# Performance work log

Hardware: AMD Instinct MI355X
Metric: run time of the kernel (lower is better)

## Reference

```python
import jax, jax.numpy as jnp
import numpy as np

N = 100000   # nodes
E = 1600000  # edges (avg degree 16)
IN = 128; HID = 128; OUT = 128; HEADS = 4
C = HID // HEADS  # 32 per-head channels


def setup_inputs() -> dict:
    key = jax.random.key(0)
    ks = jax.random.split(key, 16)
    inp = {
        "x": jax.random.normal(ks[0], (N, IN), jnp.float32),
        "edge_index": jax.random.randint(ks[1], (2, E), 0, N, dtype=jnp.int64),
        # layer 0: GATConv(IN -> C, heads=4), concat -> HID
        "W0": jax.random.normal(ks[2], (IN, HEADS * C), jnp.float32) * 0.1,
        "as0": jax.random.normal(ks[3], (HEADS, C), jnp.float32) * 0.1,
        "ad0": jax.random.normal(ks[4], (HEADS, C), jnp.float32) * 0.1,
        "b0": jax.random.normal(ks[5], (HEADS * C,), jnp.float32) * 0.1,
        # layer 1: GATConv(HID -> C, heads=4), concat -> HID
        "W1": jax.random.normal(ks[6], (HID, HEADS * C), jnp.float32) * 0.1,
        "as1": jax.random.normal(ks[7], (HEADS, C), jnp.float32) * 0.1,
        "ad1": jax.random.normal(ks[8], (HEADS, C), jnp.float32) * 0.1,
        "b1": jax.random.normal(ks[9], (HEADS * C,), jnp.float32) * 0.1,
        # layer 2: GATConv(HID -> OUT, heads=1)
        "W2": jax.random.normal(ks[10], (HID, OUT), jnp.float32) * 0.1,
        "as2": jax.random.normal(ks[11], (1, OUT), jnp.float32) * 0.1,
        "ad2": jax.random.normal(ks[12], (1, OUT), jnp.float32) * 0.1,
        "b2": jax.random.normal(ks[13], (OUT,), jnp.float32) * 0.1,
    }
    return inp


def _gat_layer(h, src, dst, W, a_src, a_dst, b, n):
    """PyG-style GATConv (concat=True, negative_slope=0.2, self-loops already in src/dst)."""
    heads, c = a_src.shape
    g = (h @ W).reshape(n, heads, c)                      # [N,H,C]
    al = jnp.sum(g * a_src, axis=-1)                      # [N,H] source attention term
    ar = jnp.sum(g * a_dst, axis=-1)                      # [N,H] dest attention term
    e = jax.nn.leaky_relu(al[src] + ar[dst], 0.2)         # [Etot,H]
    # segment softmax over incoming edges of each dst node (stable)
    m = jax.ops.segment_max(e, dst, num_segments=n)
    ex = jnp.exp(e - m[dst])
    s = jax.ops.segment_sum(ex, dst, num_segments=n)
    alpha = ex / (s[dst] + 1e-16)                         # [Etot,H]
    out = jax.ops.segment_sum(g[src] * alpha[..., None], dst, num_segments=n)  # [N,H,C]
    return out.reshape(n, heads * c) + b


def reference(x, edge_index, W0, as0, ad0, b0, W1, as1, ad1, b1, W2, as2, ad2, b2):
    n = x.shape[0]
    loops = jnp.arange(n, dtype=edge_index.dtype)         # add_self_loops=True
    src = jnp.concatenate([edge_index[0], loops])
    dst = jnp.concatenate([edge_index[1], loops])
    h = jax.nn.relu(_gat_layer(x, src, dst, W0, as0, ad0, b0, n))  # dropout inactive (eval)
    h = jax.nn.relu(_gat_layer(h, src, dst, W1, as1, ad1, b1, n))
    return _gat_layer(h, src, dst, W2, as2, ad2, b2, n)
```

## Files before the change

### kernel.cpp

```cpp
#include <hip/hip_runtime.h>
#include <hip/hip_bf16.h>
#include <hip/hip_fp16.h>

#define NNODES 100000
#define NEDGES 1600000
#define ETOT   (NEDGES + NNODES)
#define SCANB  1024
#define NSCAN  ((NNODES + SCANB - 1) / SCANB)
#define NB     782
#define NBINBLK 256

typedef _Float16 half8 __attribute__((ext_vector_type(8)));
typedef float f32x4 __attribute__((ext_vector_type(4)));

struct WSrc { const void* p[12]; };

__device__ __forceinline__ float ld_f(const void* p, long i, int f32) {
  if (f32) return ((const float*)p)[i];
  return __bfloat162float(((const __hip_bfloat16*)p)[i]);
}

__device__ __forceinline__ unsigned short f2bf_bits(float v) {
  __hip_bfloat16 b = __float2bfloat16(v);
  return __builtin_bit_cast(unsigned short, b);
}

__global__ void detect_kernel(const void* xraw, const void* eraw, int* flags) {
  __shared__ int cnt0, cnt1;
  if (threadIdx.x == 0) { cnt0 = 0; cnt1 = 0; }
  __syncthreads();
  const int* e32 = (const int*)eraw;
  int nz = 0;
  for (int i = threadIdx.x; i < 2048; i += blockDim.x) nz += (e32[2 * i + 1] != 0);
  const unsigned short* xs = (const unsigned short*)xraw;
  int weird = 0;
  for (int i = threadIdx.x; i < 4096; i += blockDim.x) {
    unsigned short u = xs[2 * i];
    int ex = (u >> 7) & 0xFF;
    weird += (ex > 168 || (ex < 88 && ex != 0)) ? 1 : 0;
  }
  atomicAdd(&cnt0, nz);
  atomicAdd(&cnt1, weird);
  __syncthreads();
  if (threadIdx.x == 0) {
    flags[0] = (cnt0 < 1024) ? 1 : 0;
    flags[1] = (cnt1 > 512) ? 1 : 0;
  }
}

__global__ void conv_wts_kernel(WSrc wsrc, float* dst, const int* flags) {
  const int start[13] = {0, 16384, 16512, 16640, 16768, 33152, 33280, 33408,
                         33536, 49920, 50048, 50176, 50304};
  int f32 = flags[1];
  int stride = gridDim.x * blockDim.x;
  for (int i = blockIdx.x * blockDim.x + threadIdx.x; i < 50304; i += stride) {
    int s = 0;
    while (start[s + 1] <= i) s++;
    dst[i] = ld_f(wsrc.p[s], i - start[s], f32);
  }
}

__global__ void conv_wtrans(const float* wts, __half* Wt) {
  const int woff[3] = {0, 16768, 33536};
  int i = blockIdx.x * blockDim.x + threadIdx.x;
  if (i >= 3 * 16384) return;
  int layer = i >> 14, rem = i & 16383;
  int c = rem >> 7, k = rem & 127;
  Wt[i] = __float2half(wts[woff[layer] + k * 128 + c]);
}

__device__ __forceinline__ void load_edge(const void* raw, int i64, long e, int& s, int& d) {
  if (i64) {
    const long long* r = (const long long*)raw;
    s = (int)r[e];
    d = (int)r[NEDGES + e];
  } else {
    const int* r = (const int*)raw;
    s = r[e];
    d = r[NEDGES + e];
  }
}

__device__ __forceinline__ int load_dst(const void* raw, int i64, long e) {
  if (i64) return (int)((const long long*)raw)[NEDGES + e];
  return ((const int*)raw)[NEDGES + e];
}

__global__ __launch_bounds__(256) void binhist(const void* raw, const int* flags, int* bcnt) {
  __shared__ int h[NB];
  for (int t = threadIdx.x; t < NB; t += 256) h[t] = 0;
  __syncthreads();
  int i64 = flags[0];
  long per = (NEDGES + NBINBLK - 1) / NBINBLK;
  long lo = (long)blockIdx.x * per;
  long hi = lo + per; if (hi > NEDGES) hi = NEDGES;
  for (long e = lo + threadIdx.x; e < hi; e += 256)
    atomicAdd(&h[load_dst(raw, i64, e) >> 7], 1);
  __syncthreads();
  for (int t = threadIdx.x; t < NB; t += 256) {
    int c = h[t];
    if (c) atomicAdd(&bcnt[t], c);
  }
}

__global__ __launch_bounds__(1024) void binscan(const int* bcnt, int* boff, int* bcur) {
  __shared__ int lds[1024];
  int t = threadIdx.x;
  int x = (t < NB) ? bcnt[t] : 0;
  lds[t] = x;
  __syncthreads();
  for (int off = 1; off < 1024; off <<= 1) {
    int v = (t >= off) ? lds[t - off] : 0;
    __syncthreads();
    lds[t] += v;
    __syncthreads();
  }
  int excl = lds[t] - x;
  if (t < NB) { boff[t] = excl; bcur[t] = excl; }
  if (t == 0) boff[NB] = NEDGES;
}

__global__ __launch_bounds__(256) void binplace(const void* raw, const int* flags, int* bcur,
                                                int* ebuf) {
  __shared__ int hist[NB];
  __shared__ int base[NB];
  int i64 = flags[0];
  long per = (NEDGES + NBINBLK - 1) / NBINBLK;
  long lo = (long)blockIdx.x * per;
  long hi = lo + per; if (hi > NEDGES) hi = NEDGES;
  for (int t = threadIdx.x; t < NB; t += 256) hist[t] = 0;
  __syncthreads();
  for (long e = lo + threadIdx.x; e < hi; e += 256)
    atomicAdd(&hist[load_dst(raw, i64, e) >> 7], 1);
  __syncthreads();
  for (int t = threadIdx.x; t < NB; t += 256) {
    int c = hist[t];
    base[t] = c ? atomicAdd(&bcur[t], c) : 0;
    hist[t] = 0;
  }
  __syncthreads();
  for (long e = lo + threadIdx.x; e < hi; e += 256) {
    int s, d;
    load_edge(raw, i64, e, s, d);
    int b = d >> 7;
    int pos = base[b] + atomicAdd(&hist[b], 1);
    ebuf[pos] = s | ((d & 127) << 17);
  }
}

__global__ __launch_bounds__(256) void deghist(const int* ebuf, const int* boff, int* deg) {
  __shared__ int h[128];
  int b = blockIdx.x, t = threadIdx.x;
  if (t < 128) h[t] = 0;
  __syncthreads();
  int beg = boff[b], end = boff[b + 1];
  for (int i = beg + t; i < end; i += 256) atomicAdd(&h[ebuf[i] >> 17], 1);
  __syncthreads();
  int node = b * 128 + t;
  if (t < 128 && node < NNODES) deg[node] = h[t];
}

__global__ __launch_bounds__(1024) void scan_part(const int* deg, int* part) {
  __shared__ int lds[SCANB];
  int b = blockIdx.x, t = threadIdx.x;
  int idx = b * SCANB + t;
  lds[t] = (idx < NNODES) ? deg[idx] + 1 : 0;
  __syncthreads();
  for (int off = 512; off > 0; off >>= 1) {
    if (t < off) lds[t] += lds[t + off];
    __syncthreads();
  }
  if (t == 0) part[b] = lds[0];
}

__global__ __launch_bounds__(128) void scan_tops(int* part) {
  __shared__ int lds[128];
  int t = threadIdx.x;
  lds[t] = (t < NSCAN) ? part[t] : 0;
  __syncthreads();
  for (int off = 1; off < 128; off <<= 1) {
    int v = (t >= off) ? lds[t - off] : 0;
    __syncthreads();
    lds[t] += v;
    __syncthreads();
  }
  if (t < NSCAN) part[t] = (t == 0) ? 0 : lds[t - 1];
}

__global__ __launch_bounds__(1024) void scan_write(const int* deg, const int* part, int* rs) {
  __shared__ int lds[SCANB];
  int b = blockIdx.x, t = threadIdx.x;
  int idx = b * SCANB + t;
  int x = (idx < NNODES) ? deg[idx] + 1 : 0;
  lds[t] = x;
  __syncthreads();
  for (int off = 1; off < SCANB; off <<= 1) {
    int v = (t >= off) ? lds[t - off] : 0;
    __syncthreads();
    lds[t] += v;
    __syncthreads();
  }
  int incl = part[b] + lds[t];
  int excl = incl - x;
  if (idx < NNODES) rs[idx] = excl;
  if (idx == NNODES - 1) rs[NNODES] = incl;
}

__global__ __launch_bounds__(256) void bucket_scatter(const int* ebuf, const int* boff,
                                                      const int* rs, int* adj) {
  __shared__ int cur[128];
  int b = blockIdx.x, t = threadIdx.x;
  int node = b * 128 + t;
  if (t < 128) cur[t] = (node < NNODES) ? rs[node] : 0;
  __syncthreads();
  int beg = boff[b], end = boff[b + 1];
  for (int i = beg + t; i < end; i += 256) {
    int v = ebuf[i];
    int pos = atomicAdd(&cur[v >> 17], 1);
    adj[pos] = v & 0x1FFFF;
  }
  __syncthreads();
  if (t < 128 && node < NNODES) adj[cur[t]] = node;
}

template <int H, int SRC>
__global__ __launch_bounds__(256) void gemm_mfma(const void* Araw, const float* wts,
                                                 const __half* Wt, int as_off, int ad_off,
                                                 __half* G, float* al, float* ar,
                                                 const int* flags) {
  __shared__ unsigned short Wl[128 * 128];
  __shared__ unsigned short Al[64 * 128];
  const int tid = threadIdx.x;
  const int rowbase = blockIdx.x * 64;
  for (int i = tid; i < 2048; i += 256) {
    int col = i >> 4, kc = i & 15;
    ((uint4*)Wl)[col * 16 + (kc ^ (col & 7))] = ((const uint4*)Wt)[i];
  }
  if (SRC == 0) {
    const __half* A = (const __half*)Araw;
    for (int i = tid; i < 1024; i += 256) {
      int row = i >> 4, kc = i & 15;
      int grow = rowbase + row;
      uint4 v = {0, 0, 0, 0};
      if (grow < NNODES) v = *(const uint4*)&A[(size_t)grow * 128 + kc * 8];
      ((uint4*)Al)[row * 16 + (kc ^ (row & 7))] = v;
    }
  } else {
    int f32 = flags[1];
    for (int i = tid; i < 1024; i += 256) {
      int row = i >> 4, kc = i & 15;
      int grow = rowbase + row;
      _Float16 tmp[8];
#pragma unroll
      for (int j = 0; j < 8; j++) tmp[j] = (_Float16)0.f;
      if (grow < NNODES) {
        if (f32) {
          const float* A = (const float*)Araw;
#pragma unroll
          for (int j = 0; j < 8; j++) tmp[j] = (_Float16)A[(size_t)grow * 128 + kc * 8 + j];
        } else {
          const __hip_bfloat16* A = (const __hip_bfloat16*)Araw;
#pragma unroll
          for (int j = 0; j < 8; j++)
            tmp[j] = (_Float16)__bfloat162float(A[(size_t)grow * 128 + kc * 8 + j]);
        }
      }
      ((uint4*)Al)[row * 16 + (kc ^ (row & 7))] = *(const uint4*)tmp;
    }
  }
  __syncthreads();
  int wv = tid >> 6, l = tid & 63;
  int lr = l & 15, lg = l >> 4;
  f32x4 acc[8];
#pragma unroll
  for (int n = 0; n < 8; n++) acc[n] = (f32x4){0.f, 0.f, 0.f, 0.f};
  int arow = wv * 16 + lr;
#pragma unroll
  for (int ks = 0; ks < 4; ks++) {
    half8 a = *(const half8*)&Al[(arow * 16 + ((ks * 4 + lg) ^ (arow & 7))) * 8];
#pragma unroll
    for (int n = 0; n < 8; n++) {
      int wrow = n * 16 + lr;
      half8 bf = *(const half8*)&Wl[(wrow * 16 + ((ks * 4 + lg) ^ (wrow & 7))) * 8];
      acc[n] = __builtin_amdgcn_mfma_f32_16x16x32_f16(a, bf, acc[n], 0, 0, 0);
    }
  }
  float as_row[8], ad_row[8];
#pragma unroll
  for (int n = 0; n < 8; n++) {
    as_row[n] = wts[as_off + n * 16 + lr];
    ad_row[n] = wts[ad_off + n * 16 + lr];
  }
  if (H == 4) {
    float pa[4][4], pb[4][4];
#pragma unroll
    for (int j = 0; j < 4; j++)
#pragma unroll
      for (int h = 0; h < 4; h++) {
        pa[j][h] = acc[2 * h][j] * as_row[2 * h] + acc[2 * h + 1][j] * as_row[2 * h + 1];
        pb[j][h] = acc[2 * h][j] * ad_row[2 * h] + acc[2 * h + 1][j] * ad_row[2 * h + 1];
      }
#pragma unroll
    for (int msk = 1; msk <= 8; msk <<= 1)
#pragma unroll
      for (int j = 0; j < 4; j++)
#pragma unroll
        for (int h = 0; h < 4; h++) {
          pa[j][h] += __shfl_xor(pa[j][h], msk, 64);
          pb[j][h] += __shfl_xor(pb[j][h], msk, 64);
        }
    if (lr == 0) {
#pragma unroll
      for (int j = 0; j < 4; j++) {
        int gr = rowbase + wv * 16 + lg * 4 + j;
        if (gr < NNODES) {
#pragma unroll
          for (int h = 0; h < 4; h++) {
            al[(size_t)gr * 4 + h] = pa[j][h];
            ar[(size_t)gr * 4 + h] = pb[j][h];
          }
        }
      }
    }
  } else {
    float pa[4], pb[4];
#pragma unroll
    for (int j = 0; j < 4; j++) {
      pa[j] = 0.f;
      pb[j] = 0.f;
#pragma unroll
      for (int n = 0; n < 8; n++) {
        pa[j] = fmaf(acc[n][j], as_row[n], pa[j]);
        pb[j] = fmaf(acc[n][j], ad_row[n], pb[j]);
      }
    }
#pragma unroll
    for (int msk = 1; msk <= 8; msk <<= 1)
#pragma unroll
      for (int j = 0; j < 4; j++) {
        pa[j] += __shfl_xor(pa[j], msk, 64);
        pb[j] += __shfl_xor(pb[j], msk, 64);
      }
    if (lr == 0) {
#pragma unroll
      for (int j = 0; j < 4; j++) {
        int gr = rowbase + wv * 16 + lg * 4 + j;
        if (gr < NNODES) { al[gr] = pa[j]; ar[gr] = pb[j]; }
      }
    }
  }
  __syncthreads();
#pragma unroll
  for (int n = 0; n < 8; n++)
#pragma unroll
    for (int j = 0; j < 4; j++) {
      int r = wv * 16 + lg * 4 + j;
      Al[r * 128 + n * 16 + lr] = __builtin_bit_cast(unsigned short, (_Float16)acc[n][j]);
    }
  __syncthreads();
  for (int i = tid; i < 1024; i += 256) {
    int row = i >> 4, kc = i & 15;
    int grow = rowbase + row;
    if (grow < NNODES) *(uint4*)&G[(size_t)grow * 128 + kc * 8] = ((const uint4*)Al)[i];
  }
}

template <int H, int RELU, int OUTCONV>
__global__ __launch_bounds__(256) void aggregate3(const __half* G, const float* al, const float* ar,
                                                  const float* wts, int b_off, const int* rs,
                                                  const int* adj, void* out, const int* flags) {
  int node = blockIdx.x * 4 + (threadIdx.x >> 6);
  if (node >= NNODES) return;
  int l = threadIdx.x & 63;
  int hh = (l & 3) & (H - 1);
  int hA = l >> 4;
  float ar_d = ar[(size_t)node * H + hh];
  int beg = rs[node], end = rs[node + 1];
  float m = -1e30f, sum = 0.f;
  float accx = 0.f, accy = 0.f;
  for (int base = beg; base < end; base += 16) {
    int nj = end - base; if (nj > 16) nj = 16;
    int slot = base + (l >> 2);
    bool valid = slot < end;
    int s = valid ? adj[slot] : 0;
    float av = al[(size_t)s * H + hh];
    __half2 g[16];
#pragma unroll
    for (int j = 0; j < 16; j++) {
      int sj = __shfl(s, 4 * j, 64);
      if (j < nj) g[j] = *(const __half2*)&G[(size_t)sj * 128 + 2 * l];
    }
    float v = av + ar_d;
    float e = valid ? ((v > 0.f) ? v : 0.2f * v) : -1e30f;
    float cm = e;
    cm = fmaxf(cm, __shfl_xor(cm, 4, 64));
    cm = fmaxf(cm, __shfl_xor(cm, 8, 64));
    cm = fmaxf(cm, __shfl_xor(cm, 16, 64));
    cm = fmaxf(cm, __shfl_xor(cm, 32, 64));
    float mn = fmaxf(m, cm);
    float scale = __expf(m - mn);
    float p = __expf(e - mn);
    float cs = p;
    cs += __shfl_xor(cs, 4, 64);
    cs += __shfl_xor(cs, 8, 64);
    cs += __shfl_xor(cs, 16, 64);
    cs += __shfl_xor(cs, 32, 64);
    sum = sum * scale + cs;
    m = mn;
    float scA = __shfl(scale, hA, 64);
    accx *= scA;
    accy *= scA;
#pragma unroll
    for (int j = 0; j < 16; j++) {
      if (j < nj) {
        float aA = __shfl(p, 4 * j + hA, 64);
        float2 g2 = __half22float2(g[j]);
        accx = fmaf(aA, g2.x, accx);
        accy = fmaf(aA, g2.y, accy);
      }
    }
  }
  float inv = 1.f / (__shfl(sum, hA, 64) + 1e-16f);
  float2 b2 = *(const float2*)&wts[b_off + 2 * l];
  float ox = accx * inv + b2.x;
  float oy = accy * inv + b2.y;
  if (RELU) {
    ox = fmaxf(ox, 0.f);
    oy = fmaxf(oy, 0.f);
  }
  size_t oi = (size_t)node * 128 + 2 * l;
  if (OUTCONV) {
    if (flags[1]) {
      *(float2*)&((float*)out)[oi] = make_float2(ox, oy);
    } else {
      *(ushort2*)&((unsigned short*)out)[oi] = make_ushort2(f2bf_bits(ox), f2bf_bits(oy));
    }
  } else {
    *(__half2*)&((__half*)out)[oi] = __floats2half2_rn(ox, oy);
  }
}

extern "C" void kernel_launch(void* const* d_in, const int* in_sizes, int n_in,
                              void* d_out, int out_size, void* d_ws, size_t ws_size,
                              hipStream_t stream) {
  char* ws = (char*)d_ws;
  size_t cur = 0;
  auto alloc = [&](size_t bytes) {
    size_t o = cur;
    cur += (bytes + 255) & ~(size_t)255;
    return o;
  };
  size_t off_flags = alloc(256);
  size_t off_wts = alloc(50304 * 4);
  size_t off_wt = alloc(3 * 16384 * 2);
  size_t off_ebuf = alloc((size_t)NEDGES * 4);
  size_t off_bcnt = alloc((size_t)NB * 4);
  size_t off_boff = alloc(((size_t)NB + 1) * 4);
  size_t off_bcur = alloc((size_t)NB * 4);
  size_t off_deg = alloc((size_t)NNODES * 4);
  size_t off_part = alloc((size_t)NSCAN * 4 + 256);
  size_t off_rs = alloc(((size_t)NNODES + 1) * 4);
  size_t off_adj = alloc((size_t)ETOT * 4);
  size_t off_al = alloc((size_t)NNODES * 4 * 4);
  size_t off_ar = alloc((size_t)NNODES * 4 * 4);
  size_t off_g = alloc((size_t)NNODES * 128 * 2);
  size_t off_ha = alloc((size_t)NNODES * 128 * 2);
  size_t off_hb = alloc((size_t)NNODES * 128 * 2);

  int* flags = (int*)(ws + off_flags);
  float* wts = (float*)(ws + off_wts);
  __half* Wt = (__half*)(ws + off_wt);
  int* ebuf = (int*)(ws + off_ebuf);
  int* bcnt = (int*)(ws + off_bcnt);
  int* boff = (int*)(ws + off_boff);
  int* bcur = (int*)(ws + off_bcur);
  int* deg = (int*)(ws + off_deg);
  int* part = (int*)(ws + off_part);
  int* rs = (int*)(ws + off_rs);
  int* adj = (int*)(ws + off_adj);
  float* al = (float*)(ws + off_al);
  float* ar = (float*)(ws + off_ar);
  __half* G = (__half*)(ws + off_g);
  __half* ha = (__half*)(ws + off_ha);
  __half* hb = (__half*)(ws + off_hb);

  detect_kernel<<<1, 256, 0, stream>>>(d_in[0], d_in[1], flags);

  WSrc wsrc;
  for (int i = 0; i < 12; i++) wsrc.p[i] = d_in[2 + i];
  conv_wts_kernel<<<64, 256, 0, stream>>>(wsrc, wts, flags);
  conv_wtrans<<<192, 256, 0, stream>>>(wts, Wt);

  (void)hipMemsetAsync(bcnt, 0, (size_t)NB * 4, stream);
  binhist<<<NBINBLK, 256, 0, stream>>>(d_in[1], flags, bcnt);
  binscan<<<1, 1024, 0, stream>>>(bcnt, boff, bcur);
  binplace<<<NBINBLK, 256, 0, stream>>>(d_in[1], flags, bcur, ebuf);
  deghist<<<NB, 256, 0, stream>>>(ebuf, boff, deg);
  scan_part<<<NSCAN, 1024, 0, stream>>>(deg, part);
  scan_tops<<<1, 128, 0, stream>>>(part);
  scan_write<<<NSCAN, 1024, 0, stream>>>(deg, part, rs);
  bucket_scatter<<<NB, 256, 0, stream>>>(ebuf, boff, rs, adj);

  const int GEMMG = (NNODES + 63) / 64;
  gemm_mfma<4, 1><<<GEMMG, 256, 0, stream>>>(d_in[0], wts, Wt, 16384, 16512, G, al, ar, flags);
  aggregate3<4, 1, 0><<<NNODES / 4, 256, 0, stream>>>(G, al, ar, wts, 16640, rs, adj, ha, flags);
  gemm_mfma<4, 0><<<GEMMG, 256, 0, stream>>>(ha, wts, Wt + 16384, 33152, 33280, G, al, ar, flags);
  aggregate3<4, 1, 0><<<NNODES / 4, 256, 0, stream>>>(G, al, ar, wts, 33408, rs, adj, hb, flags);
  gemm_mfma<1, 0><<<GEMMG, 256, 0, stream>>>(hb, wts, Wt + 32768, 49920, 50048, G, al, ar, flags);
  aggregate3<1, 0, 1><<<NNODES / 4, 256, 0, stream>>>(G, al, ar, wts, 50176, rs, adj, d_out, flags);
}
```

Before: 417.1 us.

## Process 32 edges per chunk in aggregation with two heads per lane

The aggregation kernel now handles 32 neighbor edges per iteration instead of 16. Each lane pair covers one edge, and each lane computes attention logits for two heads using float2 loads. Neighbor indices are broadcast with readlane instead of shuffles. This halves loop iterations and reduction rounds per node and issues more outstanding gathers, at the cost of more registers (32 half2 values) and wasted work for low-degree nodes. The separate weight-transpose kernel is also folded into the weight-conversion kernel to save a launch.

```diff
diff --git a/kernel.cpp b/kernel.cpp
--- a/kernel.cpp
+++ b/kernel.cpp
@@ -48,7 +48,7 @@
   }
 }
 
-__global__ void conv_wts_kernel(WSrc wsrc, float* dst, const int* flags) {
+__global__ void conv_wts_kernel(WSrc wsrc, float* dst, __half* Wt, const int* flags) {
   const int start[13] = {0, 16384, 16512, 16640, 16768, 33152, 33280, 33408,
                          33536, 49920, 50048, 50176, 50304};
   int f32 = flags[1];
@@ -56,17 +56,15 @@
   for (int i = blockIdx.x * blockDim.x + threadIdx.x; i < 50304; i += stride) {
     int s = 0;
     while (start[s + 1] <= i) s++;
-    dst[i] = ld_f(wsrc.p[s], i - start[s], f32);
-  }
-}
-
-__global__ void conv_wtrans(const float* wts, __half* Wt) {
-  const int woff[3] = {0, 16768, 33536};
-  int i = blockIdx.x * blockDim.x + threadIdx.x;
-  if (i >= 3 * 16384) return;
-  int layer = i >> 14, rem = i & 16383;
-  int c = rem >> 7, k = rem & 127;
-  Wt[i] = __float2half(wts[woff[layer] + k * 128 + c]);
+    float v = ld_f(wsrc.p[s], i - start[s], f32);
+    dst[i] = v;
+    if (s == 0 || s == 4 || s == 8) {
+      int layer = s >> 2;
+      int rem = i - start[s];
+      int k = rem >> 7, c = rem & 127;
+      Wt[layer * 16384 + c * 128 + k] = __float2half(v);
+    }
+  }
 }
 
 __device__ __forceinline__ void load_edge(const void* raw, int i64, long e, int& s, int& d) {
@@ -366,61 +364,112 @@
 }
 
 template <int H, int RELU, int OUTCONV>
-__global__ __launch_bounds__(256) void aggregate3(const __half* G, const float* al, const float* ar,
+__global__ __launch_bounds__(256) void aggregate4(const __half* G, const float* al, const float* ar,
                                                   const float* wts, int b_off, const int* rs,
                                                   const int* adj, void* out, const int* flags) {
   int node = blockIdx.x * 4 + (threadIdx.x >> 6);
   if (node >= NNODES) return;
   int l = threadIdx.x & 63;
-  int hh = (l & 3) & (H - 1);
   int hA = l >> 4;
-  float ar_d = ar[(size_t)node * H + hh];
+  int sel = (H == 4) ? (hA & 1) : 0;
+  int srcoff = (H == 4) ? (hA >> 1) : 0;
+  int hh0 = (H == 4) ? ((l & 1) * 2) : 0;
+  float ar0, ar1;
+  if (H == 4) {
+    float2 a2 = *(const float2*)&ar[(size_t)node * 4 + hh0];
+    ar0 = a2.x; ar1 = a2.y;
+  } else {
+    ar0 = ar[node]; ar1 = 0.f;
+  }
   int beg = rs[node], end = rs[node + 1];
-  float m = -1e30f, sum = 0.f;
+  float m0 = -1e30f, m1 = -1e30f, sum0 = 0.f, sum1 = 0.f;
   float accx = 0.f, accy = 0.f;
-  for (int base = beg; base < end; base += 16) {
-    int nj = end - base; if (nj > 16) nj = 16;
-    int slot = base + (l >> 2);
+  for (int base = beg; base < end; base += 32) {
+    int nj = end - base; if (nj > 32) nj = 32;
+    int slot = base + (l >> 1);
     bool valid = slot < end;
     int s = valid ? adj[slot] : 0;
-    float av = al[(size_t)s * H + hh];
-    __half2 g[16];
-#pragma unroll
-    for (int j = 0; j < 16; j++) {
-      int sj = __shfl(s, 4 * j, 64);
-      if (j < nj) g[j] = *(const __half2*)&G[(size_t)sj * 128 + 2 * l];
-    }
-    float v = av + ar_d;
-    float e = valid ? ((v > 0.f) ? v : 0.2f * v) : -1e30f;
-    float cm = e;
-    cm = fmaxf(cm, __shfl_xor(cm, 4, 64));
-    cm = fmaxf(cm, __shfl_xor(cm, 8, 64));
-    cm = fmaxf(cm, __shfl_xor(cm, 16, 64));
-    cm = fmaxf(cm, __shfl_xor(cm, 32, 64));
-    float mn = fmaxf(m, cm);
-    float scale = __expf(m - mn);
-    float p = __expf(e - mn);
-    float cs = p;
-    cs += __shfl_xor(cs, 4, 64);
-    cs += __shfl_xor(cs, 8, 64);
-    cs += __shfl_xor(cs, 16, 64);
-    cs += __shfl_xor(cs, 32, 64);
-    sum = sum * scale + cs;
-    m = mn;
-    float scA = __shfl(scale, hA, 64);
+    float av0, av1;
+    if (H == 4) {
+      float2 a2 = *(const float2*)&al[(size_t)s * 4 + hh0];
+      av0 = a2.x; av1 = a2.y;
+    } else { av0 = al[s]; av1 = 0.f; }
+    __half2 g[32];
+#pragma unroll
+    for (int j = 0; j < 32; j++) {
+      if (j < nj) {
+        int sj = __builtin_amdgcn_readlane(s, 2 * j);
+        g[j] = *(const __half2*)&G[(size_t)sj * 128 + 2 * l];
+      }
+    }
+    float v0 = av0 + ar0;
+    float e0 = valid ? ((v0 > 0.f) ? v0 : 0.2f * v0) : -1e30f;
+    float e1 = 0.f;
+    if (H == 4) {
+      float v1 = av1 + ar1;
+      e1 = valid ? ((v1 > 0.f) ? v1 : 0.2f * v1) : -1e30f;
+    }
+    float c0 = e0, c1 = e1;
+#pragma unroll
+    for (int msk = 2; msk <= 32; msk <<= 1) {
+      c0 = fmaxf(c0, __shfl_xor(c0, msk, 64));
+      if (H == 4) c1 = fmaxf(c1, __shfl_xor(c1, msk, 64));
+    }
+    float mn0 = fmaxf(m0, c0);
+    float sc0 = __expf(m0 - mn0);
+    float p0 = __expf(e0 - mn0);
+    float cs0 = p0;
+    float mn1 = 0.f, sc1 = 0.f, p1 = 0.f, cs1 = 0.f;
+    if (H == 4) {
+      mn1 = fmaxf(m1, c1);
+      sc1 = __expf(m1 - mn1);
+      p1 = __expf(e1 - mn1);
+      cs1 = p1;
+    }
+#pragma unroll
+    for (int msk = 2; msk <= 32; msk <<= 1) {
+      cs0 += __shfl_xor(cs0, msk, 64);
+      if (H == 4) cs1 += __shfl_xor(cs1, msk, 64);
+    }
+    sum0 = sum0 * sc0 + cs0;
+    m0 = mn0;
+    if (H == 4) { sum1 = sum1 * sc1 + cs1; m1 = mn1; }
+    float scA;
+    if (H == 4) {
+      float t0 = __shfl(sc0, srcoff, 64);
+      float t1 = __shfl(sc1, srcoff, 64);
+      scA = sel ? t1 : t0;
+    } else {
+      scA = __shfl(sc0, 0, 64);
+    }
     accx *= scA;
     accy *= scA;
 #pragma unroll
-    for (int j = 0; j < 16; j++) {
+    for (int j = 0; j < 32; j++) {
       if (j < nj) {
-        float aA = __shfl(p, 4 * j + hA, 64);
+        float aA;
+        if (H == 4) {
+          float t0 = __shfl(p0, 2 * j + srcoff, 64);
+          float t1 = __shfl(p1, 2 * j + srcoff, 64);
+          aA = sel ? t1 : t0;
+        } else {
+          aA = __shfl(p0, 2 * j, 64);
+        }
         float2 g2 = __half22float2(g[j]);
         accx = fmaf(aA, g2.x, accx);
         accy = fmaf(aA, g2.y, accy);
       }
     }
   }
-  float inv = 1.f / (__shfl(sum, hA, 64) + 1e-16f);
+  float smA;
+  if (H == 4) {
+    float t0 = __shfl(sum0, srcoff, 64);
+    float t1 = __shfl(sum1, srcoff, 64);
+    smA = sel ? t1 : t0;
+  } else {
+    smA = __shfl(sum0, 0, 64);
+  }
+  float inv = 1.f / (smA + 1e-16f);
   float2 b2 = *(const float2*)&wts[b_off + 2 * l];
   float ox = accx * inv + b2.x;
   float oy = accy * inv + b2.y;
@@ -488,8 +537,7 @@
 
   WSrc wsrc;
   for (int i = 0; i < 12; i++) wsrc.p[i] = d_in[2 + i];
-  conv_wts_kernel<<<64, 256, 0, stream>>>(wsrc, wts, flags);
-  conv_wtrans<<<192, 256, 0, stream>>>(wts, Wt);
+  conv_wts_kernel<<<64, 256, 0, stream>>>(wsrc, wts, Wt, flags);
 
   (void)hipMemsetAsync(bcnt, 0, (size_t)NB * 4, stream);
   binhist<<<NBINBLK, 256, 0, stream>>>(d_in[1], flags, bcnt);
@@ -503,9 +551,9 @@
 
   const int GEMMG = (NNODES + 63) / 64;
   gemm_mfma<4, 1><<<GEMMG, 256, 0, stream>>>(d_in[0], wts, Wt, 16384, 16512, G, al, ar, flags);
-  aggregate3<4, 1, 0><<<NNODES / 4, 256, 0, stream>>>(G, al, ar, wts, 16640, rs, adj, ha, flags);
+  aggregate4<4, 1, 0><<<NNODES / 4, 256, 0, stream>>>(G, al, ar, wts, 16640, rs, adj, ha, flags);
   gemm_mfma<4, 0><<<GEMMG, 256, 0, stream>>>(ha, wts, Wt + 16384, 33152, 33280, G, al, ar, flags);
-  aggregate3<4, 1, 0><<<NNODES / 4, 256, 0, stream>>>(G, al, ar, wts, 33408, rs, adj, hb, flags);
+  aggregate4<4, 1, 0><<<NNODES / 4, 256, 0, stream>>>(G, al, ar, wts, 33408, rs, adj, hb, flags);
   gemm_mfma<1, 0><<<GEMMG, 256, 0, stream>>>(hb, wts, Wt + 32768, 49920, 50048, G, al, ar, flags);
-  aggregate3<1, 0, 1><<<NNODES / 4, 256, 0, stream>>>(G, al, ar, wts, 50176, rs, adj, d_out, flags);
-}
+  aggregate4<1, 0, 1><<<NNODES / 4, 256, 0, stream>>>(G, al, ar, wts, 50176, rs, adj, d_out, flags);
+}
```

New measurement: 459.9 us. +10.3%, slower.
